# Kernel optimization log

Measured on AMD Instinct MI355X. Metric: run time of the kernel, lower is better.

The kernel has to match this reference:

```python
import jax, jax.numpy as jnp
import numpy as np

D = 4096        # hidden_dim / latent_dim
R = 512         # number of latents
H = 32          # n_heads
HD = D // H     # head_dim = 128
T = 8192        # total tokens (sum of seqlens)
EPS = 1e-5


def layernorm(x, w, b):
    mu = jnp.mean(x, axis=-1, keepdims=True)
    var = jnp.mean(jnp.square(x - mu), axis=-1, keepdims=True)
    return (x - mu) * jax.lax.rsqrt(var + EPS) * w + b


def setup_inputs() -> dict:
    key = jax.random.key(0)
    ks = jax.random.split(key, 16)
    s = 0.02
    inp = {
        'x': jax.random.normal(ks[0], (T, D), jnp.float32),
        'seqlens': jnp.full((8,), T // 8, jnp.int64) if False else jnp.full((8,), T // 8, jnp.int32),
        'latents': jax.random.normal(ks[1], (R, D), jnp.float32),
        # PreNorm layernorms (query norm on x, context norm on latents)
        'ln_q_w': 1.0 + 0.1 * jax.random.normal(ks[2], (D,), jnp.float32),
        'ln_q_b': 0.1 * jax.random.normal(ks[3], (D,), jnp.float32),
        'ln_c_w': 1.0 + 0.1 * jax.random.normal(ks[4], (D,), jnp.float32),
        'ln_c_b': 0.1 * jax.random.normal(ks[5], (D,), jnp.float32),
        # attention projections, stored (in, out) so y = x @ W
        'Wq': s * jax.random.normal(ks[6], (D, D), jnp.float32),
        'Wk': s * jax.random.normal(ks[7], (D, D), jnp.float32),
        'Wv': s * jax.random.normal(ks[8], (D, D), jnp.float32),
        'Wo': s * jax.random.normal(ks[9], (D, D), jnp.float32),
        # single PreNorm MLP block (n_layers=1)
        'ln_m_w': 1.0 + 0.1 * jax.random.normal(ks[10], (D,), jnp.float32),
        'ln_m_b': 0.1 * jax.random.normal(ks[11], (D,), jnp.float32),
        'W1': s * jax.random.normal(ks[12], (D, D), jnp.float32),
        'W2': s * jax.random.normal(ks[13], (D, D), jnp.float32),
    }
    return inp


def reference(x, seqlens, latents, ln_q_w, ln_q_b, ln_c_w, ln_c_b,
              Wq, Wk, Wv, Wo, ln_m_w, ln_m_b, W1, W2):
    # --- PreNorm cross-attention: queries = ragged tokens, KV = latents ---
    # BlockDiagonalMask(q_seqlen=seqlens, kv_seqlen=[r]*b) with identical
    # latents per block == dense attention of all tokens vs the r latents.
    xq = layernorm(x, ln_q_w, ln_q_b)                 # (T, D)
    xc = layernorm(latents, ln_c_w, ln_c_b)           # (R, D)
    q = (xq @ Wq).reshape(T, H, HD)                   # (T, H, HD)
    k = (xc @ Wk).reshape(R, H, HD)                   # (R, H, HD)
    v = (xc @ Wv).reshape(R, H, HD)
    scale = HD ** -0.5
    scores = jnp.einsum('thd,rhd->htr', q, k) * scale  # (H, T, R)
    attn = jax.nn.softmax(scores, axis=-1)
    o = jnp.einsum('htr,rhd->thd', attn, v).reshape(T, D)
    attn_out = o @ Wo                                  # (T, D)

    hiddens = attn_out + x                             # residual

    # --- PreNorm MLP block (n_layers=1) ---
    y = layernorm(hiddens, ln_m_w, ln_m_b)
    m = jax.nn.gelu(y @ W1, approximate=False) @ W2 + y  # MLP_block inner residual
    hiddens = m + hiddens                                # outer residual

    # compress_rate == -1 -> mean_mask is None, output passes through
    return hiddens
```

## Files before the change

kernel.cpp:

```cpp
#include <hip/hip_runtime.h>
#include <hip/hip_bf16.h>
#include <math.h>

#define D 4096
#define T 8192
#define R 512
#define HD 128
#define NH 32

typedef unsigned short u16;
typedef u16 u16x8 __attribute__((ext_vector_type(8)));
typedef __bf16 bf16x8 __attribute__((ext_vector_type(8)));
typedef float f32x4 __attribute__((ext_vector_type(4)));

__device__ __forceinline__ u16 f2bf(float f) {
  unsigned u = __builtin_bit_cast(unsigned, f);
  u += 0x7FFFu + ((u >> 16) & 1u);
  return (u16)(u >> 16);
}
__device__ __forceinline__ float bf2f(u16 b) {
  return __builtin_bit_cast(float, ((unsigned)b) << 16);
}
__device__ __forceinline__ bf16x8 ldb8(const u16* p) {
  return __builtin_bit_cast(bf16x8, *(const u16x8*)p);
}
__device__ __forceinline__ void async_cp16(void* gsrc, void* ldst) {
  typedef __attribute__((address_space(1))) void gvoid;
  typedef __attribute__((address_space(3))) void lvoid;
  __builtin_amdgcn_global_load_lds((gvoid*)gsrc, (lvoid*)ldst, 16, 0, 0);
}
#define MFMA(a, b, c) __builtin_amdgcn_mfma_f32_16x16x32_bf16(a, b, c, 0, 0, 0)

__device__ __forceinline__ void wg_barrier() {
  asm volatile("" ::: "memory");
  __builtin_amdgcn_s_barrier();
  asm volatile("" ::: "memory");
}

__global__ __launch_bounds__(256) void ln_bf16(
    const float* __restrict__ X, const float* __restrict__ w,
    const float* __restrict__ b, u16* __restrict__ out) {
  const int row = blockIdx.x, tid = threadIdx.x;
  const int lane = tid & 63, wv = tid >> 6;
  const float* xr = X + (long)row * D;
  float4 v[4];
  float s = 0.f, ss = 0.f;
#pragma unroll
  for (int i = 0; i < 4; ++i) {
    v[i] = *(const float4*)(xr + tid * 4 + i * 1024);
    s += v[i].x + v[i].y + v[i].z + v[i].w;
    ss += v[i].x * v[i].x + v[i].y * v[i].y + v[i].z * v[i].z + v[i].w * v[i].w;
  }
#pragma unroll
  for (int off = 32; off >= 1; off >>= 1) {
    s += __shfl_xor(s, off);
    ss += __shfl_xor(ss, off);
  }
  __shared__ float sw[4], ssw[4];
  if (lane == 0) { sw[wv] = s; ssw[wv] = ss; }
  __syncthreads();
  s = sw[0] + sw[1] + sw[2] + sw[3];
  ss = ssw[0] + ssw[1] + ssw[2] + ssw[3];
  const float mu = s * (1.f / D);
  const float var = ss * (1.f / D) - mu * mu;
  const float rstd = rsqrtf(var + 1e-5f);
#pragma unroll
  for (int i = 0; i < 4; ++i) {
    const int base = tid * 4 + i * 1024;
    const float4 wv4 = *(const float4*)(w + base);
    const float4 bv4 = *(const float4*)(b + base);
    ushort4 ov;
    ov.x = f2bf((v[i].x - mu) * rstd * wv4.x + bv4.x);
    ov.y = f2bf((v[i].y - mu) * rstd * wv4.y + bv4.y);
    ov.z = f2bf((v[i].z - mu) * rstd * wv4.z + bv4.z);
    ov.w = f2bf((v[i].w - mu) * rstd * wv4.w + bv4.w);
    *(ushort4*)(out + (long)row * D + base) = ov;
  }
}

__global__ __launch_bounds__(256) void wconv(const float* __restrict__ W,
                                             u16* __restrict__ Wt) {
  __shared__ float t[32][33];
  const int tx = threadIdx.x & 31, ty = threadIdx.x >> 5;
  const int n0 = blockIdx.x * 32, k0 = blockIdx.y * 32;
#pragma unroll
  for (int i = 0; i < 4; ++i)
    t[ty + i * 8][tx] = W[(long)(k0 + ty + i * 8) * D + n0 + tx];
  __syncthreads();
#pragma unroll
  for (int i = 0; i < 4; ++i)
    Wt[(long)(n0 + ty + i * 8) * D + k0 + tx] = f2bf(t[tx][ty + i * 8]);
}

template <int EPI>
__global__ __launch_bounds__(256) void gemm_bt(
    const u16* __restrict__ A, const u16* __restrict__ Bt, u16* __restrict__ ob,
    u16* __restrict__ ob2, float* __restrict__ of, const float* __restrict__ af,
    const u16* __restrict__ ab, float scale) {
  __shared__ u16 As[128 * 32];
  __shared__ u16 Bs[128 * 32];
  const int tid = threadIdx.x;
  const int bx = blockIdx.x, by = blockIdx.y;
  const int lane = tid & 63, w = tid >> 6;
  const int ln15 = lane & 15, q = lane >> 4;
  const int wm = (w >> 1) * 64, wn = (w & 1) * 64;

  const int c0 = tid, c1 = tid + 256;
  const u16* ag0 = A + (long)(by * 128 + (c0 >> 2)) * D + (c0 & 3) * 8;
  const u16* ag1 = A + (long)(by * 128 + (c1 >> 2)) * D + (c1 & 3) * 8;
  const u16* bg0 = Bt + (long)(bx * 128 + (c0 >> 2)) * D + (c0 & 3) * 8;
  const u16* bg1 = Bt + (long)(bx * 128 + (c1 >> 2)) * D + (c1 & 3) * 8;
  u16* al0 = As + (tid & ~63) * 8;
  u16* al1 = As + ((tid & ~63) + 256) * 8;
  u16* bl0 = Bs + (tid & ~63) * 8;
  u16* bl1 = Bs + ((tid & ~63) + 256) * 8;

  f32x4 acc[4][4];
#pragma unroll
  for (int i = 0; i < 4; ++i)
#pragma unroll
    for (int j = 0; j < 4; ++j) {
      f32x4 z = {0.f, 0.f, 0.f, 0.f};
      acc[i][j] = z;
    }

  for (int k0 = 0; k0 < D; k0 += 32) {
    __syncthreads();
    async_cp16((void*)(ag0 + k0), al0);
    async_cp16((void*)(ag1 + k0), al1);
    async_cp16((void*)(bg0 + k0), bl0);
    async_cp16((void*)(bg1 + k0), bl1);
    __syncthreads();
    bf16x8 av[4], bv[4];
#pragma unroll
    for (int i = 0; i < 4; ++i) av[i] = ldb8(As + (wm + i * 16 + ln15) * 32 + q * 8);
#pragma unroll
    for (int j = 0; j < 4; ++j) bv[j] = ldb8(Bs + (wn + j * 16 + ln15) * 32 + q * 8);
#pragma unroll
    for (int i = 0; i < 4; ++i)
#pragma unroll
      for (int j = 0; j < 4; ++j) acc[i][j] = MFMA(av[i], bv[j], acc[i][j]);
  }

#pragma unroll
  for (int i = 0; i < 4; ++i) {
    const int gmb = by * 128 + wm + i * 16 + q * 4;
#pragma unroll
    for (int j = 0; j < 4; ++j) {
      const int gn = bx * 128 + wn + j * 16 + ln15;
#pragma unroll
      for (int r = 0; r < 4; ++r) {
        const int gm = gmb + r;
        const float vacc = acc[i][j][r];
        const long idx = (long)gm * D + gn;
        if constexpr (EPI == 1) {
          if (gn < D)
            ob[idx] = f2bf(vacc);
          else
            ob2[(long)(gn - D) * R + gm] = f2bf(vacc);
        } else {
          ob[idx] = f2bf(vacc * scale);
        }
      }
    }
  }
}

template <int MG>
__device__ __forceinline__ void readA(bf16x8 (&bA)[2][4], const u16* aB,
                                      int base, int cc0, int cc1) {
#pragma unroll
  for (int im = 0; im < 4; ++im) {
    bA[0][im] = ldb8(aB + (MG * 4 + im) * 1024 + base + cc0);
    bA[1][im] = ldb8(aB + (MG * 4 + im) * 1024 + base + cc1);
  }
}
template <int NJ0>
__device__ __forceinline__ void readB(bf16x8 (&bB)[2][4], const u16* bP,
                                      int base, int cc0, int cc1) {
#pragma unroll
  for (int nj = 0; nj < 2; ++nj) {
    bB[0][NJ0 + nj] = ldb8(bP + (NJ0 + nj) * 1024 + base + cc0);
    bB[1][NJ0 + nj] = ldb8(bP + (NJ0 + nj) * 1024 + base + cc1);
  }
}
template <int MG, int NJ0>
__device__ __forceinline__ void mfma16(f32x4 (&acc)[8][4], const bf16x8 (&bA)[2][4],
                                       const bf16x8 (&bB)[2][4]) {
#pragma unroll
  for (int im = 0; im < 4; ++im)
#pragma unroll
    for (int nj = 0; nj < 2; ++nj)
#pragma unroll
      for (int kk = 0; kk < 2; ++kk)
        acc[MG * 4 + im][NJ0 + nj] =
            MFMA(bA[kk][im], bB[kk][NJ0 + nj], acc[MG * 4 + im][NJ0 + nj]);
}

template <int EPI>
__global__ __launch_bounds__(512, 2) void gemm256(
    const u16* __restrict__ A, const u16* __restrict__ Bt, u16* __restrict__ ob,
    float* __restrict__ of, const float* __restrict__ af,
    const u16* __restrict__ ab, float scale) {
  __shared__ u16 As[2][2][8192];
  __shared__ u16 Bs[2][2][8192];
  const int tid = threadIdx.x;
  const int bx = blockIdx.x, by = blockIdx.y;
  const int lane = tid & 63, w = tid >> 6;
  const int ln15 = lane & 15, q = lane >> 4;
  const int wm = w >> 2, wn = w & 3;

  const int r0 = tid >> 3, s0 = (tid & 7) ^ (r0 & 7);
  const int r1 = 64 + r0, s1 = (tid & 7) ^ (r1 & 7);
  const long oA00 = (long)(by * 256 + r0) * D + s0 * 8;
  const long oA01 = (long)(by * 256 + r1) * D + s1 * 8;
  const long oA10 = (long)(by * 256 + 128 + r0) * D + s0 * 8;
  const long oA11 = (long)(by * 256 + 128 + r1) * D + s1 * 8;
  const long oB00 = (long)(bx * 256 + r0) * D + s0 * 8;
  const long oB01 = (long)(bx * 256 + r1) * D + s1 * 8;
  const long oB10 = (long)(bx * 256 + 128 + r0) * D + s0 * 8;
  const long oB11 = (long)(bx * 256 + 128 + r1) * D + s1 * 8;
  const int d0 = w * 512, d1 = 4096 + w * 512;

  const int sw = ln15 & 7;
  const int cc0 = (q ^ sw) * 8;
  const int cc1 = ((4 + q) ^ sw) * 8;
  const int baseA = ln15 * 64;
  const int baseB = (wn & 1) * 4096 + ln15 * 64;

  f32x4 acc[8][4];
#pragma unroll
  for (int i = 0; i < 8; ++i)
#pragma unroll
    for (int j = 0; j < 4; ++j) {
      f32x4 z = {0.f, 0.f, 0.f, 0.f};
      acc[i][j] = z;
    }

  auto stageA = [&](int buf, int kt) {
    async_cp16((void*)(A + oA00 + kt * 64), &As[buf][0][d0]);
    async_cp16((void*)(A + oA01 + kt * 64), &As[buf][0][d1]);
    async_cp16((void*)(A + oA10 + kt * 64), &As[buf][1][d0]);
    async_cp16((void*)(A + oA11 + kt * 64), &As[buf][1][d1]);
  };
  auto stageB = [&](int buf, int kt) {
    async_cp16((void*)(Bt + oB00 + kt * 64), &Bs[buf][0][d0]);
    async_cp16((void*)(Bt + oB01 + kt * 64), &Bs[buf][0][d1]);
    async_cp16((void*)(Bt + oB10 + kt * 64), &Bs[buf][1][d0]);
    async_cp16((void*)(Bt + oB11 + kt * 64), &Bs[buf][1][d1]);
  };

  stageA(0, 0);
  stageB(0, 0);
  asm volatile("s_waitcnt vmcnt(0)" ::: "memory");
  wg_barrier();

  int cur = 0;
  for (int t = 0; t < D / 64; ++t) {
    const int nxt = cur ^ 1;
    const bool pf = (t + 1 < D / 64);
    const u16* aB = &As[cur][wm][0];
    const u16* bP = &Bs[cur][wn >> 1][0];
    bf16x8 bA[2][4], bB[2][4];
    readA<0>(bA, aB, baseA, cc0, cc1);
    readB<0>(bB, bP, baseB, cc0, cc1);
    if (pf) stageA(nxt, t + 1);
    wg_barrier();
    asm volatile("s_waitcnt lgkmcnt(0)" ::: "memory");
    __builtin_amdgcn_s_setprio(1);
    mfma16<0, 0>(acc, bA, bB);
    __builtin_amdgcn_s_setprio(0);
    wg_barrier();
    readB<2>(bB, bP, baseB, cc0, cc1);
    if (pf) stageB(nxt, t + 1);
    wg_barrier();
    asm volatile("s_waitcnt lgkmcnt(0)" ::: "memory");
    __builtin_amdgcn_s_setprio(1);
    mfma16<0, 2>(acc, bA, bB);
    __builtin_amdgcn_s_setprio(0);
    wg_barrier();
    readA<1>(bA, aB, baseA, cc0, cc1);
    wg_barrier();
    asm volatile("s_waitcnt lgkmcnt(0)" ::: "memory");
    __builtin_amdgcn_s_setprio(1);
    mfma16<1, 0>(acc, bA, bB);
    __builtin_amdgcn_s_setprio(0);
    wg_barrier();
    __builtin_amdgcn_s_setprio(1);
    mfma16<1, 2>(acc, bA, bB);
    __builtin_amdgcn_s_setprio(0);
    asm volatile("s_waitcnt vmcnt(0)" ::: "memory");
    wg_barrier();
    cur = nxt;
  }

#pragma unroll
  for (int mi = 0; mi < 8; ++mi) {
    const int gmb = by * 256 + wm * 128 + mi * 16 + q * 4;
#pragma unroll
    for (int nj = 0; nj < 4; ++nj) {
      const int gn = bx * 256 + wn * 64 + nj * 16 + ln15;
#pragma unroll
      for (int r = 0; r < 4; ++r) {
        const int gm = gmb + r;
        const float vacc = acc[mi][nj][r];
        const long idx = (long)gm * D + gn;
        if constexpr (EPI == 0) {
          ob[idx] = f2bf(vacc * scale);
        } else if constexpr (EPI == 2) {
          of[idx] = vacc + af[idx];
        } else if constexpr (EPI == 3) {
          ob[idx] = f2bf(0.5f * vacc * (1.f + erff(vacc * 0.7071067811865475f)));
        } else {
          of[idx] = of[idx] + vacc + bf2f(ab[idx]);
        }
      }
    }
  }
}

__global__ __launch_bounds__(256) void attn_fused(const u16* Q,
                                                  const u16* __restrict__ Kb,
                                                  const u16* __restrict__ Vt,
                                                  u16* O) {
  __shared__ u16 Qs[64 * 136];
  __shared__ u16 Ks[64 * 136];
  __shared__ u16 Vs[128 * 72];
  __shared__ u16 Ps[4][16 * 72];
  const int tid = threadIdx.x;
  const int lane = tid & 63, w = tid >> 6;
  const int ln15 = lane & 15, q = lane >> 4;
  const int t0 = blockIdx.x * 64, h = blockIdx.y;

#pragma unroll
  for (int it = 0; it < 4; ++it) {
    const int c = tid + it * 256;
    const int row = c >> 4, cj = c & 15;
    *(u16x8*)(Qs + row * 136 + cj * 8) =
        *(const u16x8*)(Q + (long)(t0 + row) * D + h * HD + cj * 8);
  }

  f32x4 o[8];
  float m_run[4], l_run[4];
#pragma unroll
  for (int t = 0; t < 8; ++t) {
    f32x4 z = {0.f, 0.f, 0.f, 0.f};
    o[t] = z;
  }
#pragma unroll
  for (int r = 0; r < 4; ++r) {
    m_run[r] = -1e30f;
    l_run[r] = 0.f;
  }

  for (int ch = 0; ch < 8; ++ch) {
    const int r0 = ch * 64;
    __syncthreads();
#pragma unroll
    for (int it = 0; it < 4; ++it) {
      const int c = tid + it * 256;
      const int row = c >> 4, cj = c & 15;
      *(u16x8*)(Ks + row * 136 + cj * 8) =
          *(const u16x8*)(Kb + (long)(r0 + row) * D + h * HD + cj * 8);
    }
#pragma unroll
    for (int it = 0; it < 4; ++it) {
      const int c = tid + it * 256;
      const int hd = c >> 3, rj = c & 7;
      *(u16x8*)(Vs + hd * 72 + rj * 8) =
          *(const u16x8*)(Vt + (long)(h * HD + hd) * R + r0 + rj * 8);
    }
    __syncthreads();

    f32x4 s[4];
#pragma unroll
    for (int j = 0; j < 4; ++j) {
      f32x4 z = {0.f, 0.f, 0.f, 0.f};
      s[j] = z;
    }
#pragma unroll
    for (int kk = 0; kk < 4; ++kk) {
      const bf16x8 a = ldb8(Qs + (w * 16 + ln15) * 136 + kk * 32 + q * 8);
#pragma unroll
      for (int j = 0; j < 4; ++j) {
        const bf16x8 b = ldb8(Ks + (j * 16 + ln15) * 136 + kk * 32 + q * 8);
        s[j] = MFMA(a, b, s[j]);
      }
    }
    float mx[4], rs[4];
#pragma unroll
    for (int r = 0; r < 4; ++r)
      mx[r] = fmaxf(fmaxf(s[0][r], s[1][r]), fmaxf(s[2][r], s[3][r]));
#pragma unroll
    for (int off = 8; off >= 1; off >>= 1)
#pragma unroll
      for (int r = 0; r < 4; ++r) mx[r] = fmaxf(mx[r], __shfl_xor(mx[r], off));
#pragma unroll
    for (int r = 0; r < 4; ++r) {
      const float mn = fmaxf(m_run[r], mx[r]);
      const float al = __expf(m_run[r] - mn);
      m_run[r] = mn;
      float a2 = 0.f;
#pragma unroll
      for (int j = 0; j < 4; ++j) {
        const float p = __expf(s[j][r] - mn);
        s[j][r] = p;
        a2 += p;
      }
      rs[r] = a2;
      l_run[r] *= al;
#pragma unroll
      for (int t = 0; t < 8; ++t) o[t][r] *= al;
    }
#pragma unroll
    for (int off = 8; off >= 1; off >>= 1)
#pragma unroll
      for (int r = 0; r < 4; ++r) rs[r] += __shfl_xor(rs[r], off);
#pragma unroll
    for (int r = 0; r < 4; ++r) l_run[r] += rs[r];
#pragma unroll
    for (int j = 0; j < 4; ++j)
#pragma unroll
      for (int r = 0; r < 4; ++r)
        Ps[w][(q * 4 + r) * 72 + j * 16 + ln15] = f2bf(s[j][r]);
    __syncthreads();
#pragma unroll
    for (int kk = 0; kk < 2; ++kk) {
      const bf16x8 a = ldb8(Ps[w] + ln15 * 72 + kk * 32 + q * 8);
#pragma unroll
      for (int t = 0; t < 8; ++t) {
        const bf16x8 b = ldb8(Vs + (t * 16 + ln15) * 72 + kk * 32 + q * 8);
        o[t] = MFMA(a, b, o[t]);
      }
    }
  }
#pragma unroll
  for (int r = 0; r < 4; ++r) l_run[r] = 1.f / l_run[r];
#pragma unroll
  for (int t = 0; t < 8; ++t)
#pragma unroll
    for (int r = 0; r < 4; ++r) {
      const int row = t0 + w * 16 + q * 4 + r;
      const int col = h * HD + t * 16 + ln15;
      O[(long)row * D + col] = f2bf(o[t][r] * l_run[r]);
    }
}

extern "C" void kernel_launch(void* const* d_in, const int* in_sizes, int n_in,
                              void* d_out, int out_size, void* d_ws, size_t ws_size,
                              hipStream_t stream) {
  (void)in_sizes; (void)n_in; (void)out_size;
  const float* x      = (const float*)d_in[0];
  const float* lat    = (const float*)d_in[2];
  const float* ln_q_w = (const float*)d_in[3];
  const float* ln_q_b = (const float*)d_in[4];
  const float* ln_c_w = (const float*)d_in[5];
  const float* ln_c_b = (const float*)d_in[6];
  const float* Wq     = (const float*)d_in[7];
  const float* Wk     = (const float*)d_in[8];
  const float* Wv     = (const float*)d_in[9];
  const float* Wo     = (const float*)d_in[10];
  const float* ln_m_w = (const float*)d_in[11];
  const float* ln_m_b = (const float*)d_in[12];
  const float* W1     = (const float*)d_in[13];
  const float* W2     = (const float*)d_in[14];
  float* out = (float*)d_out;

  const long DD = (long)D * D, TD = (long)T * D, RD = (long)R * D;
  u16* p = (u16*)d_ws;
  u16* Wt   = p; p += 2 * DD;
  u16* a_bf = p; p += TD;
  u16* q_bf = p; p += TD;
  u16* xc   = p; p += RD;
  u16* k_bf = p; p += RD;
  u16* v_t  = p; p += RD;
  if (ws_size < (size_t)(p - (u16*)d_ws) * sizeof(u16)) return;

  const dim3 B(256);
  const dim3 B5(512);
  const dim3 Gw(128, 128);
  const dim3 Gg(16, 32);

  ln_bf16<<<T, B, 0, stream>>>(x, ln_q_w, ln_q_b, a_bf);
  ln_bf16<<<R, B, 0, stream>>>(lat, ln_c_w, ln_c_b, xc);

  wconv<<<Gw, B, 0, stream>>>(Wq, Wt);
  gemm256<0><<<Gg, B5, 0, stream>>>(a_bf, Wt, q_bf, nullptr, nullptr, nullptr,
                                    0.08838834764831845f);

  wconv<<<Gw, B, 0, stream>>>(Wk, Wt);
  wconv<<<Gw, B, 0, stream>>>(Wv, Wt + DD);
  gemm_bt<1><<<dim3(64, 4), B, 0, stream>>>(xc, Wt, k_bf, v_t, nullptr, nullptr,
                                            nullptr, 1.f);

  attn_fused<<<dim3(128, 32), B, 0, stream>>>(q_bf, k_bf, v_t, q_bf);

  wconv<<<Gw, B, 0, stream>>>(Wo, Wt);
  gemm256<2><<<Gg, B5, 0, stream>>>(q_bf, Wt, nullptr, out, x, nullptr, 1.f);

  ln_bf16<<<T, B, 0, stream>>>(out, ln_m_w, ln_m_b, a_bf);

  wconv<<<Gw, B, 0, stream>>>(W1, Wt);
  gemm256<3><<<Gg, B5, 0, stream>>>(a_bf, Wt, q_bf, nullptr, nullptr, nullptr, 1.f);

  wconv<<<Gw, B, 0, stream>>>(W2, Wt);
  gemm256<4><<<Gg, B5, 0, stream>>>(q_bf, Wt, nullptr, out, nullptr, a_bf, 1.f);
}
```

Baseline: 1.986 ms.

## Prefetch two k-tiles ahead in gemm256 and restructure main loop into two k-halves

The main GEMM loop now issues async global-to-LDS copies two k-tiles ahead instead of one, and waits with a partial vmcnt so the next tile can still be in flight. The four-phase read/MFMA schedule with six barriers per iteration becomes two phases (k-half cc0, then cc1) with two barriers. This is meant to hide global load latency better and cut synchronisation. The cost is more registers for the fragment arrays, and the buffer reuse is fragile because the stage for t+2 overwrites the current buffer after only one barrier.

```diff
diff --git a/kernel.cpp b/kernel.cpp
--- a/kernel.cpp
+++ b/kernel.cpp
@@ -166,37 +166,6 @@
   }
 }
 
-template <int MG>
-__device__ __forceinline__ void readA(bf16x8 (&bA)[2][4], const u16* aB,
-                                      int base, int cc0, int cc1) {
-#pragma unroll
-  for (int im = 0; im < 4; ++im) {
-    bA[0][im] = ldb8(aB + (MG * 4 + im) * 1024 + base + cc0);
-    bA[1][im] = ldb8(aB + (MG * 4 + im) * 1024 + base + cc1);
-  }
-}
-template <int NJ0>
-__device__ __forceinline__ void readB(bf16x8 (&bB)[2][4], const u16* bP,
-                                      int base, int cc0, int cc1) {
-#pragma unroll
-  for (int nj = 0; nj < 2; ++nj) {
-    bB[0][NJ0 + nj] = ldb8(bP + (NJ0 + nj) * 1024 + base + cc0);
-    bB[1][NJ0 + nj] = ldb8(bP + (NJ0 + nj) * 1024 + base + cc1);
-  }
-}
-template <int MG, int NJ0>
-__device__ __forceinline__ void mfma16(f32x4 (&acc)[8][4], const bf16x8 (&bA)[2][4],
-                                       const bf16x8 (&bB)[2][4]) {
-#pragma unroll
-  for (int im = 0; im < 4; ++im)
-#pragma unroll
-    for (int nj = 0; nj < 2; ++nj)
-#pragma unroll
-      for (int kk = 0; kk < 2; ++kk)
-        acc[MG * 4 + im][NJ0 + nj] =
-            MFMA(bA[kk][im], bB[kk][NJ0 + nj], acc[MG * 4 + im][NJ0 + nj]);
-}
-
 template <int EPI>
 __global__ __launch_bounds__(512, 2) void gemm256(
     const u16* __restrict__ A, const u16* __restrict__ Bt, u16* __restrict__ ob,
@@ -250,48 +219,57 @@
     async_cp16((void*)(Bt + oB11 + kt * 64), &Bs[buf][1][d1]);
   };
 
+  const int NT = D / 64;
   stageA(0, 0);
   stageB(0, 0);
-  asm volatile("s_waitcnt vmcnt(0)" ::: "memory");
+  stageA(1, 1);
+  stageB(1, 1);
+  asm volatile("s_waitcnt vmcnt(8)" ::: "memory");
   wg_barrier();
 
   int cur = 0;
-  for (int t = 0; t < D / 64; ++t) {
-    const int nxt = cur ^ 1;
-    const bool pf = (t + 1 < D / 64);
+  for (int t = 0; t < NT; ++t) {
+    const bool pf = (t + 2 < NT);
     const u16* aB = &As[cur][wm][0];
     const u16* bP = &Bs[cur][wn >> 1][0];
-    bf16x8 bA[2][4], bB[2][4];
-    readA<0>(bA, aB, baseA, cc0, cc1);
-    readB<0>(bB, bP, baseB, cc0, cc1);
-    if (pf) stageA(nxt, t + 1);
+
+    bf16x8 a0[8], b0[4];
+#pragma unroll
+    for (int im = 0; im < 8; ++im) a0[im] = ldb8(aB + im * 1024 + baseA + cc0);
+#pragma unroll
+    for (int nj = 0; nj < 4; ++nj) b0[nj] = ldb8(bP + nj * 1024 + baseB + cc0);
+    __builtin_amdgcn_s_setprio(1);
+#pragma unroll
+    for (int im = 0; im < 8; ++im)
+#pragma unroll
+      for (int nj = 0; nj < 4; ++nj) acc[im][nj] = MFMA(a0[im], b0[nj], acc[im][nj]);
+    __builtin_amdgcn_s_setprio(0);
+
+    bf16x8 a1[8], b1[4];
+#pragma unroll
+    for (int im = 0; im < 8; ++im) a1[im] = ldb8(aB + im * 1024 + baseA + cc1);
+#pragma unroll
+    for (int nj = 0; nj < 4; ++nj) b1[nj] = ldb8(bP + nj * 1024 + baseB + cc1);
+    asm volatile("s_waitcnt lgkmcnt(0)" ::: "memory");
     wg_barrier();
-    asm volatile("s_waitcnt lgkmcnt(0)" ::: "memory");
+
+    if (pf) {
+      stageA(cur, t + 2);
+      stageB(cur, t + 2);
+    }
     __builtin_amdgcn_s_setprio(1);
-    mfma16<0, 0>(acc, bA, bB);
+#pragma unroll
+    for (int im = 0; im < 8; ++im)
+#pragma unroll
+      for (int nj = 0; nj < 4; ++nj) acc[im][nj] = MFMA(a1[im], b1[nj], acc[im][nj]);
     __builtin_amdgcn_s_setprio(0);
+
+    if (pf)
+      asm volatile("s_waitcnt vmcnt(8)" ::: "memory");
+    else
+      asm volatile("s_waitcnt vmcnt(0)" ::: "memory");
     wg_barrier();
-    readB<2>(bB, bP, baseB, cc0, cc1);
-    if (pf) stageB(nxt, t + 1);
-    wg_barrier();
-    asm volatile("s_waitcnt lgkmcnt(0)" ::: "memory");
-    __builtin_amdgcn_s_setprio(1);
-    mfma16<0, 2>(acc, bA, bB);
-    __builtin_amdgcn_s_setprio(0);
-    wg_barrier();
-    readA<1>(bA, aB, baseA, cc0, cc1);
-    wg_barrier();
-    asm volatile("s_waitcnt lgkmcnt(0)" ::: "memory");
-    __builtin_amdgcn_s_setprio(1);
-    mfma16<1, 0>(acc, bA, bB);
-    __builtin_amdgcn_s_setprio(0);
-    wg_barrier();
-    __builtin_amdgcn_s_setprio(1);
-    mfma16<1, 2>(acc, bA, bB);
-    __builtin_amdgcn_s_setprio(0);
-    asm volatile("s_waitcnt vmcnt(0)" ::: "memory");
-    wg_barrier();
-    cur = nxt;
+    cur ^= 1;
   }
 
 #pragma unroll
```

Result: no change. 1.977 ms (-0.4%).
